# Kernel tuning notes

Hardware: AMD Instinct MI355X
Metric: run time of the kernel (lower is better)

## Reference

```python
import jax, jax.numpy as jnp
import numpy as np

B, S, D = 4, 8192, 1024

def setup_inputs() -> dict:
    key = jax.random.key(0)
    k1, k2, k3 = jax.random.split(key, 3)
    x = jax.random.normal(k1, (B, S, D), dtype=jnp.float32)
    # learned params (small random values so the op is non-trivial; torch init is zeros)
    log_scale = jax.random.normal(k2, (D,), dtype=jnp.float32) * 0.02
    theta = jax.random.normal(k3, (D,), dtype=jnp.float32) * 0.02
    return {"x": x, "log_scale": log_scale, "theta": theta}

def _rotation_cascade(x, theta):
    """Sequential Givens rotations: step i rotates coords (i, (i+1) % d).

    Key structural fact: after step i, coordinate i is final (except coord 0,
    which is touched again by the last wrap-around step). So instead of the
    original O(d) full-tensor clones, we scan with a per-batch-element scalar
    carry = current value at position i.
    """
    d = x.shape[-1]
    cos = jnp.cos(theta)
    sin = jnp.sin(theta)
    xT = jnp.moveaxis(x, -1, 0)  # [d, B, S]

    def body(carry, inp):
        c, s, r = inp                 # carry = value at pos i, r = x[..., i+1]
        out_i = c * carry - s * r     # final value at position i (for i >= 1)
        new_carry = s * carry + c * r # value at position i+1 going into step i+1
        return new_carry, out_i

    carry, outs = jax.lax.scan(body, xT[0], (cos[:-1], sin[:-1], xT[1:]))
    # last step (index d-1) rotates positions (d-1, 0); current pos-0 value is outs[0]
    new_last = cos[-1] * carry - sin[-1] * outs[0]
    new_first = sin[-1] * carry + cos[-1] * outs[0]
    yT = jnp.concatenate([new_first[None], outs[1:], new_last[None]], axis=0)
    return jnp.moveaxis(yT, 0, -1)

def reference(x, log_scale, theta):
    x_scaled = x * jnp.exp(log_scale)
    return _rotation_cascade(x_scaled, theta) - x
```

## Files before the change

kernel.cpp:

```cpp
#include <hip/hip_runtime.h>
#include <math.h>

#define D 1024

__global__ void rsa_make_tables(const float* __restrict__ log_scale,
                                const float* __restrict__ theta,
                                float* __restrict__ tab) {
    int i = blockIdx.x * blockDim.x + threadIdx.x;
    if (i < D) {
        float t = theta[i];
        float c = cosf(t), s = sinf(t);
        float scn = expf(log_scale[(i + 1) & (D - 1)]);
        tab[i]         = c;
        tab[D + i]     = s;
        tab[2 * D + i] = c * scn;
        tab[3 * D + i] = s * scn;
        if (i == 0) tab[4 * D] = expf(log_scale[0]);
    }
}

__global__ __launch_bounds__(256, 4) void rsa_rot_kernel(
    const float* __restrict__ x,
    const float* __restrict__ tab,
    float* __restrict__ out,
    int nrows)
{
    const int lane = threadIdx.x & 63;
    const int wave = threadIdx.x >> 6;
    const int row  = blockIdx.x * 4 + wave;
    if (row >= nrows) return;

    const float* xrow = x + (size_t)row * D;
    const int    off  = lane * 4;

    float4 xq[4], cq[4], sq[4], csq[4], ssq[4];
    #pragma unroll
    for (int c = 0; c < 4; ++c)
        xq[c] = *reinterpret_cast<const float4*>(xrow + c * 256 + off);
    #pragma unroll
    for (int c = 0; c < 4; ++c) {
        cq[c]  = *reinterpret_cast<const float4*>(tab +         c * 256 + off);
        sq[c]  = *reinterpret_cast<const float4*>(tab +     D + c * 256 + off);
        csq[c] = *reinterpret_cast<const float4*>(tab + 2 * D + c * 256 + off);
        ssq[c] = *reinterpret_cast<const float4*>(tab + 3 * D + c * 256 + off);
    }
    const float sc0 = tab[4 * D];
    __builtin_amdgcn_sched_barrier(0);

    float xnb[4];
    #pragma unroll
    for (int c = 0; c < 4; ++c) {
        float nb = __shfl(xq[c].x, (lane + 1) & 63);
        if (c < 3) {
            float bc = __shfl(xq[c + 1].x, 0);
            nb = (lane == 63) ? bc : nb;
        }
        xnb[c] = nb;
    }
    const float carry0 = sc0 * __shfl(xq[0].x, 0);

    float A[4], Bv[4];
    #pragma unroll
    for (int c = 0; c < 4; ++c) {
        float a = 1.0f, b = 0.0f;
        b = fmaf(sq[c].x, b, csq[c].x * xq[c].y); a *= sq[c].x;
        b = fmaf(sq[c].y, b, csq[c].y * xq[c].z); a *= sq[c].y;
        b = fmaf(sq[c].z, b, csq[c].z * xq[c].w); a *= sq[c].z;
        b = fmaf(sq[c].w, b, csq[c].w * xnb[c]);  a *= sq[c].w;
        A[c] = a; Bv[c] = b;
    }

    #pragma unroll
    for (int d = 1; d < 64; d <<= 1) {
        float Ar[4], Br[4];
        #pragma unroll
        for (int c = 0; c < 4; ++c) { Ar[c] = __shfl_up(A[c], d); Br[c] = __shfl_up(Bv[c], d); }
        if (lane >= d) {
            #pragma unroll
            for (int c = 0; c < 4; ++c) { Bv[c] = fmaf(A[c], Br[c], Bv[c]); A[c] *= Ar[c]; }
        }
    }

    float e[4];
    e[0] = carry0;
    {
        float Ga = 1.0f, Gb = 0.0f;
        #pragma unroll
        for (int c = 1; c < 4; ++c) {
            float Fa = __shfl(A[c - 1], 63), Fb = __shfl(Bv[c - 1], 63);
            Gb = fmaf(Fa, Gb, Fb);
            Ga = Fa * Ga;
            e[c] = fmaf(Ga, carry0, Gb);
        }
    }

    float carry[4];
    #pragma unroll
    for (int c = 0; c < 4; ++c) {
        float Ap = __shfl_up(A[c], 1), Bp = __shfl_up(Bv[c], 1);
        carry[c] = (lane == 0) ? e[c] : fmaf(Ap, e[c], Bp);
    }

    const float c_0  = __shfl(cq[0].x, 0);
    const float ss_0 = __shfl(ssq[0].x, 0);
    const float x_1  = __shfl(xq[0].y, 0);
    const float out0 = fmaf(c_0, carry0, -(ss_0 * x_1));

    float nf = 0.0f;
    #pragma unroll
    for (int c = 0; c < 4; ++c) {
        float cr = carry[c];
        float y0 = fmaf(cq[c].x, cr, -(ssq[c].x * xq[c].y));
        cr       = fmaf(sq[c].x, cr,   csq[c].x * xq[c].y);
        float y1 = fmaf(cq[c].y, cr, -(ssq[c].y * xq[c].z));
        cr       = fmaf(sq[c].y, cr,   csq[c].y * xq[c].z);
        float y2 = fmaf(cq[c].z, cr, -(ssq[c].z * xq[c].w));
        cr       = fmaf(sq[c].z, cr,   csq[c].z * xq[c].w);
        float xl  = xnb[c];
        float mss = ssq[c].w, mcs = csq[c].w;
        if (c == 3) {
            xl  = (lane == 63) ? out0     : xl;
            mss = (lane == 63) ? sq[c].w  : mss;
            mcs = (lane == 63) ? cq[c].w  : mcs;
        }
        float y3 = fmaf(cq[c].w, cr, -(mss * xl));
        cr       = fmaf(sq[c].w, cr,   mcs * xl);
        if (c == 3) nf = cr;
        xq[c].x = y0 - xq[c].x;
        xq[c].y = y1 - xq[c].y;
        xq[c].z = y2 - xq[c].z;
        xq[c].w = y3 - xq[c].w;
    }
    nf = __shfl(nf, 63);
    if (lane == 0) xq[0].x = (nf - out0) + xq[0].x;

    float* orow = out + (size_t)row * D;
    #pragma unroll
    for (int c = 0; c < 4; ++c)
        *reinterpret_cast<float4*>(orow + c * 256 + off) = xq[c];
}

extern "C" void kernel_launch(void* const* d_in, const int* in_sizes, int n_in,
                              void* d_out, int out_size, void* d_ws, size_t ws_size,
                              hipStream_t stream) {
    const float* x         = (const float*)d_in[0];
    const float* log_scale = (const float*)d_in[1];
    const float* theta     = (const float*)d_in[2];
    float* outp = (float*)d_out;
    float* tab  = (float*)d_ws;

    const int nrows = in_sizes[0] / D;

    rsa_make_tables<<<(D + 255) / 256, 256, 0, stream>>>(log_scale, theta, tab);

    const int blocks = (nrows + 3) / 4;
    rsa_rot_kernel<<<blocks, 256, 0, stream>>>(x, tab, outp, nrows);
}
```

Before: 49.89 us.

## Fuse table precompute into rotation kernel and recompute sin/cos/exp per wave

Drops the separate table-building kernel launch. Each wave now loads theta and log_scale directly and computes cos/sin/exp with fast intrinsics, then pre-scales x by exp(log_scale) so the folded c*scale/s*scale tables are no longer needed. This saves a launch and cuts table loads from four arrays to two. In exchange every wave repeats the transcendental math, and the fast intrinsics are less accurate.

After: 44.73 us. 10.3% less time.

```diff
diff --git a/kernel.cpp b/kernel.cpp
--- a/kernel.cpp
+++ b/kernel.cpp
@@ -3,25 +3,10 @@
 
 #define D 1024
 
-__global__ void rsa_make_tables(const float* __restrict__ log_scale,
-                                const float* __restrict__ theta,
-                                float* __restrict__ tab) {
-    int i = blockIdx.x * blockDim.x + threadIdx.x;
-    if (i < D) {
-        float t = theta[i];
-        float c = cosf(t), s = sinf(t);
-        float scn = expf(log_scale[(i + 1) & (D - 1)]);
-        tab[i]         = c;
-        tab[D + i]     = s;
-        tab[2 * D + i] = c * scn;
-        tab[3 * D + i] = s * scn;
-        if (i == 0) tab[4 * D] = expf(log_scale[0]);
-    }
-}
-
 __global__ __launch_bounds__(256, 4) void rsa_rot_kernel(
     const float* __restrict__ x,
-    const float* __restrict__ tab,
+    const float* __restrict__ log_scale,
+    const float* __restrict__ theta,
     float* __restrict__ out,
     int nrows)
 {
@@ -33,40 +18,56 @@
     const float* xrow = x + (size_t)row * D;
     const int    off  = lane * 4;
 
-    float4 xq[4], cq[4], sq[4], csq[4], ssq[4];
+    float4 thq[4], lsq[4];
+    #pragma unroll
+    for (int c = 0; c < 4; ++c) {
+        thq[c] = *reinterpret_cast<const float4*>(theta     + c * 256 + off);
+        lsq[c] = *reinterpret_cast<const float4*>(log_scale + c * 256 + off);
+    }
+    float4 xq[4];
     #pragma unroll
     for (int c = 0; c < 4; ++c)
         xq[c] = *reinterpret_cast<const float4*>(xrow + c * 256 + off);
+    __builtin_amdgcn_sched_barrier(0);
+
+    float4 cq[4], sq[4], eq[4];
     #pragma unroll
     for (int c = 0; c < 4; ++c) {
-        cq[c]  = *reinterpret_cast<const float4*>(tab +         c * 256 + off);
-        sq[c]  = *reinterpret_cast<const float4*>(tab +     D + c * 256 + off);
-        csq[c] = *reinterpret_cast<const float4*>(tab + 2 * D + c * 256 + off);
-        ssq[c] = *reinterpret_cast<const float4*>(tab + 3 * D + c * 256 + off);
+        cq[c].x = __cosf(thq[c].x); sq[c].x = __sinf(thq[c].x); eq[c].x = __expf(lsq[c].x);
+        cq[c].y = __cosf(thq[c].y); sq[c].y = __sinf(thq[c].y); eq[c].y = __expf(lsq[c].y);
+        cq[c].z = __cosf(thq[c].z); sq[c].z = __sinf(thq[c].z); eq[c].z = __expf(lsq[c].z);
+        cq[c].w = __cosf(thq[c].w); sq[c].w = __sinf(thq[c].w); eq[c].w = __expf(lsq[c].w);
     }
-    const float sc0 = tab[4 * D];
-    __builtin_amdgcn_sched_barrier(0);
+
+    float4 xsq[4];
+    #pragma unroll
+    for (int c = 0; c < 4; ++c) {
+        xsq[c].x = eq[c].x * xq[c].x;
+        xsq[c].y = eq[c].y * xq[c].y;
+        xsq[c].z = eq[c].z * xq[c].z;
+        xsq[c].w = eq[c].w * xq[c].w;
+    }
 
     float xnb[4];
     #pragma unroll
     for (int c = 0; c < 4; ++c) {
-        float nb = __shfl(xq[c].x, (lane + 1) & 63);
+        float nb = __shfl(xsq[c].x, (lane + 1) & 63);
         if (c < 3) {
-            float bc = __shfl(xq[c + 1].x, 0);
+            float bc = __shfl(xsq[c + 1].x, 0);
             nb = (lane == 63) ? bc : nb;
         }
         xnb[c] = nb;
     }
-    const float carry0 = sc0 * __shfl(xq[0].x, 0);
+    const float carry0 = __shfl(xsq[0].x, 0);
 
     float A[4], Bv[4];
     #pragma unroll
     for (int c = 0; c < 4; ++c) {
         float a = 1.0f, b = 0.0f;
-        b = fmaf(sq[c].x, b, csq[c].x * xq[c].y); a *= sq[c].x;
-        b = fmaf(sq[c].y, b, csq[c].y * xq[c].z); a *= sq[c].y;
-        b = fmaf(sq[c].z, b, csq[c].z * xq[c].w); a *= sq[c].z;
-        b = fmaf(sq[c].w, b, csq[c].w * xnb[c]);  a *= sq[c].w;
+        b = fmaf(sq[c].x, b, cq[c].x * xsq[c].y); a *= sq[c].x;
+        b = fmaf(sq[c].y, b, cq[c].y * xsq[c].z); a *= sq[c].y;
+        b = fmaf(sq[c].z, b, cq[c].z * xsq[c].w); a *= sq[c].z;
+        b = fmaf(sq[c].w, b, cq[c].w * xnb[c]);   a *= sq[c].w;
         A[c] = a; Bv[c] = b;
     }
 
@@ -102,29 +103,24 @@
     }
 
     const float c_0  = __shfl(cq[0].x, 0);
-    const float ss_0 = __shfl(ssq[0].x, 0);
-    const float x_1  = __shfl(xq[0].y, 0);
-    const float out0 = fmaf(c_0, carry0, -(ss_0 * x_1));
+    const float s_0  = __shfl(sq[0].x, 0);
+    const float xs_1 = __shfl(xsq[0].y, 0);
+    const float out0 = fmaf(c_0, carry0, -(s_0 * xs_1));
 
     float nf = 0.0f;
     #pragma unroll
     for (int c = 0; c < 4; ++c) {
         float cr = carry[c];
-        float y0 = fmaf(cq[c].x, cr, -(ssq[c].x * xq[c].y));
-        cr       = fmaf(sq[c].x, cr,   csq[c].x * xq[c].y);
-        float y1 = fmaf(cq[c].y, cr, -(ssq[c].y * xq[c].z));
-        cr       = fmaf(sq[c].y, cr,   csq[c].y * xq[c].z);
-        float y2 = fmaf(cq[c].z, cr, -(ssq[c].z * xq[c].w));
-        cr       = fmaf(sq[c].z, cr,   csq[c].z * xq[c].w);
-        float xl  = xnb[c];
-        float mss = ssq[c].w, mcs = csq[c].w;
-        if (c == 3) {
-            xl  = (lane == 63) ? out0     : xl;
-            mss = (lane == 63) ? sq[c].w  : mss;
-            mcs = (lane == 63) ? cq[c].w  : mcs;
-        }
-        float y3 = fmaf(cq[c].w, cr, -(mss * xl));
-        cr       = fmaf(sq[c].w, cr,   mcs * xl);
+        float y0 = fmaf(cq[c].x, cr, -(sq[c].x * xsq[c].y));
+        cr       = fmaf(sq[c].x, cr,   cq[c].x * xsq[c].y);
+        float y1 = fmaf(cq[c].y, cr, -(sq[c].y * xsq[c].z));
+        cr       = fmaf(sq[c].y, cr,   cq[c].y * xsq[c].z);
+        float y2 = fmaf(cq[c].z, cr, -(sq[c].z * xsq[c].w));
+        cr       = fmaf(sq[c].z, cr,   cq[c].z * xsq[c].w);
+        float xl = xnb[c];
+        if (c == 3) xl = (lane == 63) ? out0 : xl;
+        float y3 = fmaf(cq[c].w, cr, -(sq[c].w * xl));
+        cr       = fmaf(sq[c].w, cr,   cq[c].w * xl);
         if (c == 3) nf = cr;
         xq[c].x = y0 - xq[c].x;
         xq[c].y = y1 - xq[c].y;
@@ -147,12 +143,9 @@
     const float* log_scale = (const float*)d_in[1];
     const float* theta     = (const float*)d_in[2];
     float* outp = (float*)d_out;
-    float* tab  = (float*)d_ws;
 
     const int nrows = in_sizes[0] / D;
 
-    rsa_make_tables<<<(D + 255) / 256, 256, 0, stream>>>(log_scale, theta, tab);
-
     const int blocks = (nrows + 3) / 4;
-    rsa_rot_kernel<<<blocks, 256, 0, stream>>>(x, tab, outp, nrows);
+    rsa_rot_kernel<<<blocks, 256, 0, stream>>>(x, log_scale, theta, outp, nrows);
 }
```
